# Kernel optimization log

Hardware: AMD Instinct MI355X
Metric: run time of the kernel (lower is better)

## Reference

```python
import jax, jax.numpy as jnp
import numpy as np

BATCH, SEQ, EMBED = 1048576, 1, 32
HIDDEN, LAYERS = 32, 5


def setup_inputs() -> dict:
    key = jax.random.key(0)
    ks = jax.random.split(key, 7)
    s = 1.0 / np.sqrt(HIDDEN)  # PyTorch-style uniform-ish scale via scaled normals
    return {
        "x": jax.random.normal(ks[0], (BATCH, SEQ, EMBED), dtype=jnp.float32),
        "w_ih": jax.random.normal(ks[1], (LAYERS, 3 * HIDDEN, EMBED), dtype=jnp.float32) * s,
        "w_hh": jax.random.normal(ks[2], (LAYERS, 3 * HIDDEN, HIDDEN), dtype=jnp.float32) * s,
        "b_ih": jax.random.normal(ks[3], (LAYERS, 3 * HIDDEN), dtype=jnp.float32) * s,
        "b_hh": jax.random.normal(ks[4], (LAYERS, 3 * HIDDEN), dtype=jnp.float32) * s,
        "fc_w": jax.random.normal(ks[5], (EMBED, HIDDEN)) * s,  # Linear(hidden, embed): (out, in)
        "fc_b": jax.random.normal(ks[6], (EMBED,)) * s,
    }


def _gru_layer(x_tbh, h0, w_ih_l, w_hh_l, b_ih_l, b_hh_l):
    """x_tbh: (T, B, in). Returns all hidden states (T, B, H)."""
    def step(h, x_t):
        gi = x_t @ w_ih_l.T + b_ih_l          # (B, 3H)
        gh = h @ w_hh_l.T + b_hh_l            # (B, 3H)
        i_r, i_z, i_n = jnp.split(gi, 3, axis=-1)
        h_r, h_z, h_n = jnp.split(gh, 3, axis=-1)
        r = jax.nn.sigmoid(i_r + h_r)
        z = jax.nn.sigmoid(i_z + h_z)
        n = jnp.tanh(i_n + r * h_n)
        h_new = (1.0 - z) * n + z * h
        return h_new, h_new
    _, ys = jax.lax.scan(step, h0, x_tbh)
    return ys


def reference(x, w_ih, w_hh, b_ih, b_hh, fc_w, fc_b):
    B = x.shape[0]
    seq = jnp.transpose(x, (1, 0, 2))  # (T, B, E), batch_first -> time-major
    h0 = jnp.zeros((B, HIDDEN), dtype=x.dtype)
    for l in range(LAYERS):  # fixed small layer count
        seq = _gru_layer(seq, h0, w_ih[l], w_hh[l], b_ih[l], b_hh[l])
    out = jnp.transpose(seq, (1, 0, 2)).reshape(B, -1)  # (B, T*H) == (B, H) since T=1
    return out @ fc_w.T + fc_b
```

## Files before the change

### kernel.cpp

```cpp
#include <hip/hip_runtime.h>


typedef __attribute__((ext_vector_type(8))) _Float16 f16x8;
typedef __attribute__((ext_vector_type(4))) float f32x4;
typedef __attribute__((ext_vector_type(2))) float f32x2;
typedef __attribute__((ext_vector_type(4))) unsigned int u32x4;

#define NLAYER 5
#define NT     512

__device__ __forceinline__ float fexp2(float x) {
#if __has_builtin(__builtin_amdgcn_exp2f)
    return __builtin_amdgcn_exp2f(x);
#else
    return exp2f(x);
#endif
}
__device__ __forceinline__ float frcp(float x) {
#if __has_builtin(__builtin_amdgcn_rcpf)
    return __builtin_amdgcn_rcpf(x);
#else
    return 1.0f / x;
#endif
}

__device__ __forceinline__ unsigned cvt2(float f0, float f1) {
    unsigned r;
    asm("v_cvt_pkrtz_f16_f32 %0, %1, %2" : "=v"(r) : "v"(f0), "v"(f1));
    return r;
}

__device__ __forceinline__ f32x4 mfma16h(f16x8 a, f16x8 b, f32x4 c) {
    return __builtin_amdgcn_mfma_f32_16x16x32_f16(a, b, c, 0, 0, 0);
}

__device__ __forceinline__ void xpose_pair(unsigned &x, unsigned &y) {
    asm("v_permlane32_swap_b32 %0, %1" : "+v"(x), "+v"(y));
    asm("v_permlane16_swap_b32 %0, %1" : "+v"(x), "+v"(y));
}

__device__ __forceinline__ f32x2 mk2(float a, float b) { f32x2 v; v.x = a; v.y = b; return v; }
__device__ __forceinline__ f32x2 exp2v(f32x2 v) { f32x2 r; r.x = fexp2(v.x); r.y = fexp2(v.y); return r; }
__device__ __forceinline__ f32x2 rcpv(f32x2 v)  { f32x2 r; r.x = frcp(v.x);  r.y = frcp(v.y);  return r; }

__device__ __forceinline__ f32x2 gru_act2(f32x2 ar, f32x2 az, f32x2 an, f32x2 cn) {
    f32x2 er  = exp2v(ar);
    f32x2 ez  = exp2v(az);
    f32x2 r   = rcpv(er + 1.0f);
    f32x2 a2  = an + r * cn;
    f32x2 en  = exp2v(a2);
    f32x2 num = ez - ez * en;
    f32x2 den = (ez + 1.0f) * (en + 1.0f);
    return num * rcpv(den);
}

struct __align__(16) Lds {
    _Float16 wA[NLAYER * 96 * 32];
    float bsum[NLAYER * 96];
    float cn_[NLAYER * 32];
};

union BU { u32x4 w; f16x8 v; };

__global__ __launch_bounds__(NT, 5) void gru_fused(
    const float* __restrict__ x, const float* __restrict__ w_ih,
    const float* __restrict__ b_ih, const float* __restrict__ b_hh,
    const float* __restrict__ fc_w, const float* __restrict__ fc_b,
    float* __restrict__ out, int nPairs)
{
    __shared__ Lds s;
    const int tid = threadIdx.x;
    const float NL2E = -1.4426950408889634f;

    for (int i = tid; i < NLAYER * 96 * 32; i += NT) {
        int r = i >> 5;
        int g = r % 96;
        float sc = (g < 64) ? NL2E : 2.0f * NL2E;
        s.wA[i ^ ((r & 7) << 3)] = (_Float16)(w_ih[i] * sc);
    }
    for (int i = tid; i < NLAYER * 96; i += NT) {
        int c = i % 96;
        float v = b_ih[i] + (c < 64 ? b_hh[i] : 0.0f);
        s.bsum[i] = v * ((c < 64) ? NL2E : 2.0f * NL2E);
    }
    for (int i = tid; i < NLAYER * 32; i += NT) {
        int l = i >> 5, c = i & 31;
        s.cn_[i] = b_hh[l * 96 + 64 + c] * (2.0f * NL2E);
    }
    __syncthreads();

    const int lane = tid & 63;
    const int n0 = lane & 15;
    const int q  = lane >> 4;
    const int aBase = ((n0 * 32) + q * 8) ^ ((n0 & 7) << 3);

    f16x8 F0, F1;
    {
        const float* p0 = fc_w + (size_t)(n0 * 32 + q * 8);
        const float* p1 = fc_w + (size_t)((16 + n0) * 32 + q * 8);
        f32x4 a0 = *(const f32x4*)p0, a1 = *(const f32x4*)(p0 + 4);
        f32x4 b0 = *(const f32x4*)p1, b1 = *(const f32x4*)(p1 + 4);
        BU U0, U1;
        U0.w[0] = cvt2(a0[0], a0[1]); U0.w[1] = cvt2(a0[2], a0[3]);
        U0.w[2] = cvt2(a1[0], a1[1]); U0.w[3] = cvt2(a1[2], a1[3]);
        U1.w[0] = cvt2(b0[0], b0[1]); U1.w[1] = cvt2(b0[2], b0[3]);
        U1.w[2] = cvt2(b1[0], b1[1]); U1.w[3] = cvt2(b1[2], b1[3]);
        F0 = U0.v; F1 = U1.v;
    }
    f32x4 OB0 = *(const f32x4*)(fc_b + q * 4);
    f32x4 OB1 = *(const f32x4*)(fc_b + 16 + q * 4);

    const int waveId  = (int)((blockIdx.x * (unsigned)NT + tid) >> 6);
    const int nWavesG = (int)((gridDim.x * (unsigned)NT) >> 6);

    for (int t = waveId; t < nPairs; t += nWavesG) {
        const int rowBase = t * 32;

        const float* xpA = x + (size_t)(rowBase + n0) * 32 + q * 8;
        const float* xpB = x + (size_t)(rowBase + 16 + n0) * 32 + q * 8;
        f32x4 xaA = *(const f32x4*)xpA, xbA = *(const f32x4*)(xpA + 4);
        f32x4 xaB = *(const f32x4*)xpB, xbB = *(const f32x4*)(xpB + 4);
        BU BA, BB;
        BA.w[0] = cvt2(xaA[0], xaA[1]); BA.w[1] = cvt2(xaA[2], xaA[3]);
        BA.w[2] = cvt2(xbA[0], xbA[1]); BA.w[3] = cvt2(xbA[2], xbA[3]);
        BB.w[0] = cvt2(xaB[0], xaB[1]); BB.w[1] = cvt2(xaB[2], xaB[3]);
        BB.w[2] = cvt2(xbB[0], xbB[1]); BB.w[3] = cvt2(xbB[2], xbB[3]);
        f16x8 bA = BA.v, bB = BB.v;

        #pragma unroll
        for (int l = 0; l < NLAYER; ++l) {
            const _Float16* wb = s.wA + l * 96 * 32;
            const float* bs = s.bsum + l * 96;

            f32x4 cR0A, cR1A, cZ0A, cZ1A, cN0A, cN1A;
            f32x4 cR0B, cR1B, cZ0B, cZ1B, cN0B, cN1B;

            {
                f16x8 a = *(const f16x8*)(wb + aBase + 0 * 512);
                f32x4 cb = *(const f32x4*)(bs + 0 + q * 4);
                cR0A = mfma16h(a, bA, cb);
                cR0B = mfma16h(a, bB, cb);
            }
            {
                f16x8 a = *(const f16x8*)(wb + aBase + 1 * 512);
                f32x4 cb = *(const f32x4*)(bs + 16 + q * 4);
                cR1A = mfma16h(a, bA, cb);
                cR1B = mfma16h(a, bB, cb);
            }
            {
                f16x8 a = *(const f16x8*)(wb + aBase + 2 * 512);
                f32x4 cb = *(const f32x4*)(bs + 32 + q * 4);
                cZ0A = mfma16h(a, bA, cb);
                cZ0B = mfma16h(a, bB, cb);
            }
            {
                f16x8 a = *(const f16x8*)(wb + aBase + 3 * 512);
                f32x4 cb = *(const f32x4*)(bs + 48 + q * 4);
                cZ1A = mfma16h(a, bA, cb);
                cZ1B = mfma16h(a, bB, cb);
            }
            {
                f16x8 a = *(const f16x8*)(wb + aBase + 4 * 512);
                f32x4 cb = *(const f32x4*)(bs + 64 + q * 4);
                cN0A = mfma16h(a, bA, cb);
                cN0B = mfma16h(a, bB, cb);
            }
            {
                f16x8 a = *(const f16x8*)(wb + aBase + 5 * 512);
                f32x4 cb = *(const f32x4*)(bs + 80 + q * 4);
                cN1A = mfma16h(a, bA, cb);
                cN1B = mfma16h(a, bB, cb);
            }

            f32x4 vc0 = *(const f32x4*)(s.cn_ + l * 32 + 0  + q * 4);
            f32x4 vc1 = *(const f32x4*)(s.cn_ + l * 32 + 16 + q * 4);

            {
                f32x2 hA = gru_act2(mk2(cR0A[0], cR0A[1]), mk2(cZ0A[0], cZ0A[1]),
                                    mk2(cN0A[0], cN0A[1]), mk2(vc0[0], vc0[1]));
                f32x2 hB = gru_act2(mk2(cR0A[2], cR0A[3]), mk2(cZ0A[2], cZ0A[3]),
                                    mk2(cN0A[2], cN0A[3]), mk2(vc0[2], vc0[3]));
                f32x2 hC = gru_act2(mk2(cR1A[0], cR1A[1]), mk2(cZ1A[0], cZ1A[1]),
                                    mk2(cN1A[0], cN1A[1]), mk2(vc1[0], vc1[1]));
                f32x2 hD = gru_act2(mk2(cR1A[2], cR1A[3]), mk2(cZ1A[2], cZ1A[3]),
                                    mk2(cN1A[2], cN1A[3]), mk2(vc1[2], vc1[3]));
                unsigned hw0 = cvt2(hA.x, hA.y);
                unsigned hw1 = cvt2(hB.x, hB.y);
                unsigned hw2 = cvt2(hC.x, hC.y);
                unsigned hw3 = cvt2(hD.x, hD.y);
                xpose_pair(hw0, hw2);
                xpose_pair(hw1, hw3);
                BA.w[0] = hw0; BA.w[1] = hw1; BA.w[2] = hw2; BA.w[3] = hw3;
                bA = BA.v;
            }
            {
                f32x2 hA = gru_act2(mk2(cR0B[0], cR0B[1]), mk2(cZ0B[0], cZ0B[1]),
                                    mk2(cN0B[0], cN0B[1]), mk2(vc0[0], vc0[1]));
                f32x2 hB = gru_act2(mk2(cR0B[2], cR0B[3]), mk2(cZ0B[2], cZ0B[3]),
                                    mk2(cN0B[2], cN0B[3]), mk2(vc0[2], vc0[3]));
                f32x2 hC = gru_act2(mk2(cR1B[0], cR1B[1]), mk2(cZ1B[0], cZ1B[1]),
                                    mk2(cN1B[0], cN1B[1]), mk2(vc1[0], vc1[1]));
                f32x2 hD = gru_act2(mk2(cR1B[2], cR1B[3]), mk2(cZ1B[2], cZ1B[3]),
                                    mk2(cN1B[2], cN1B[3]), mk2(vc1[2], vc1[3]));
                unsigned hw0 = cvt2(hA.x, hA.y);
                unsigned hw1 = cvt2(hB.x, hB.y);
                unsigned hw2 = cvt2(hC.x, hC.y);
                unsigned hw3 = cvt2(hD.x, hD.y);
                xpose_pair(hw0, hw2);
                xpose_pair(hw1, hw3);
                BB.w[0] = hw0; BB.w[1] = hw1; BB.w[2] = hw2; BB.w[3] = hw3;
                bB = BB.v;
            }
        }

        f32x4 o0A = mfma16h(F0, bA, OB0);
        f32x4 o1A = mfma16h(F1, bA, OB1);
        f32x4 o0B = mfma16h(F0, bB, OB0);
        f32x4 o1B = mfma16h(F1, bB, OB1);

        float* opA = out + (size_t)(rowBase + n0) * 32;
        float* opB = out + (size_t)(rowBase + 16 + n0) * 32;
        *(f32x4*)(opA + 0  + q * 4) = o0A;
        *(f32x4*)(opA + 16 + q * 4) = o1A;
        *(f32x4*)(opB + 0  + q * 4) = o0B;
        *(f32x4*)(opB + 16 + q * 4) = o1B;
    }
}

extern "C" void kernel_launch(void* const* d_in, const int* in_sizes, int n_in,
                              void* d_out, int out_size, void* d_ws, size_t ws_size,
                              hipStream_t stream) {
    (void)n_in; (void)d_ws; (void)ws_size; (void)out_size;
    const float* x    = (const float*)d_in[0];
    const float* w_ih = (const float*)d_in[1];
    const float* b_ih = (const float*)d_in[3];
    const float* b_hh = (const float*)d_in[4];
    const float* fc_w = (const float*)d_in[5];
    const float* fc_b = (const float*)d_in[6];
    float* out = (float*)d_out;

    const int batch  = in_sizes[0] / 32;
    const int nPairs = batch / 32;

    gru_fused<<<1024, NT, 0, stream>>>(x, w_ih, b_ih, b_hh, fc_w, fc_b, out, nPairs);
}
```

Before: 111.0 us.

## Process one 16-row tile per wave and move FC weights to LDS

Each wave now handles one 16-row tile per iteration instead of two interleaved tiles, which halves the accumulator and activation register footprint. Launch bounds rise from 5 to 8 waves-per-EU hint. The FC weights and bias move from per-lane registers into LDS. The aim is to trade the ILP of two independent tiles for higher occupancy. It adds an LDS reload of the FC weights on every tile and loses the overlap between the two tiles' MFMA and transcendental work.

```diff
diff --git a/kernel.cpp b/kernel.cpp
--- a/kernel.cpp
+++ b/kernel.cpp
@@ -56,17 +56,19 @@
 
 struct __align__(16) Lds {
     _Float16 wA[NLAYER * 96 * 32];
+    _Float16 wF[32 * 32];
     float bsum[NLAYER * 96];
     float cn_[NLAYER * 32];
+    float fb_[32];
 };
 
 union BU { u32x4 w; f16x8 v; };
 
-__global__ __launch_bounds__(NT, 5) void gru_fused(
+__global__ __launch_bounds__(NT, 8) void gru_fused(
     const float* __restrict__ x, const float* __restrict__ w_ih,
     const float* __restrict__ b_ih, const float* __restrict__ b_hh,
     const float* __restrict__ fc_w, const float* __restrict__ fc_b,
-    float* __restrict__ out, int nPairs)
+    float* __restrict__ out, int nTiles)
 {
     __shared__ Lds s;
     const int tid = threadIdx.x;
@@ -78,6 +80,10 @@
         float sc = (g < 64) ? NL2E : 2.0f * NL2E;
         s.wA[i ^ ((r & 7) << 3)] = (_Float16)(w_ih[i] * sc);
     }
+    for (int i = tid; i < 32 * 32; i += NT) {
+        int r = i >> 5;
+        s.wF[i ^ ((r & 7) << 3)] = (_Float16)fc_w[i];
+    }
     for (int i = tid; i < NLAYER * 96; i += NT) {
         int c = i % 96;
         float v = b_ih[i] + (c < 64 ? b_hh[i] : 0.0f);
@@ -87,6 +93,7 @@
         int l = i >> 5, c = i & 31;
         s.cn_[i] = b_hh[l * 96 + 64 + c] * (2.0f * NL2E);
     }
+    if (tid < 32) s.fb_[tid] = fc_b[tid];
     __syncthreads();
 
     const int lane = tid & 63;
@@ -94,136 +101,89 @@
     const int q  = lane >> 4;
     const int aBase = ((n0 * 32) + q * 8) ^ ((n0 & 7) << 3);
 
-    f16x8 F0, F1;
-    {
-        const float* p0 = fc_w + (size_t)(n0 * 32 + q * 8);
-        const float* p1 = fc_w + (size_t)((16 + n0) * 32 + q * 8);
-        f32x4 a0 = *(const f32x4*)p0, a1 = *(const f32x4*)(p0 + 4);
-        f32x4 b0 = *(const f32x4*)p1, b1 = *(const f32x4*)(p1 + 4);
-        BU U0, U1;
-        U0.w[0] = cvt2(a0[0], a0[1]); U0.w[1] = cvt2(a0[2], a0[3]);
-        U0.w[2] = cvt2(a1[0], a1[1]); U0.w[3] = cvt2(a1[2], a1[3]);
-        U1.w[0] = cvt2(b0[0], b0[1]); U1.w[1] = cvt2(b0[2], b0[3]);
-        U1.w[2] = cvt2(b1[0], b1[1]); U1.w[3] = cvt2(b1[2], b1[3]);
-        F0 = U0.v; F1 = U1.v;
-    }
-    f32x4 OB0 = *(const f32x4*)(fc_b + q * 4);
-    f32x4 OB1 = *(const f32x4*)(fc_b + 16 + q * 4);
-
     const int waveId  = (int)((blockIdx.x * (unsigned)NT + tid) >> 6);
     const int nWavesG = (int)((gridDim.x * (unsigned)NT) >> 6);
 
-    for (int t = waveId; t < nPairs; t += nWavesG) {
-        const int rowBase = t * 32;
-
-        const float* xpA = x + (size_t)(rowBase + n0) * 32 + q * 8;
-        const float* xpB = x + (size_t)(rowBase + 16 + n0) * 32 + q * 8;
-        f32x4 xaA = *(const f32x4*)xpA, xbA = *(const f32x4*)(xpA + 4);
-        f32x4 xaB = *(const f32x4*)xpB, xbB = *(const f32x4*)(xpB + 4);
-        BU BA, BB;
-        BA.w[0] = cvt2(xaA[0], xaA[1]); BA.w[1] = cvt2(xaA[2], xaA[3]);
-        BA.w[2] = cvt2(xbA[0], xbA[1]); BA.w[3] = cvt2(xbA[2], xbA[3]);
-        BB.w[0] = cvt2(xaB[0], xaB[1]); BB.w[1] = cvt2(xaB[2], xaB[3]);
-        BB.w[2] = cvt2(xbB[0], xbB[1]); BB.w[3] = cvt2(xbB[2], xbB[3]);
-        f16x8 bA = BA.v, bB = BB.v;
+    for (int t = waveId; t < nTiles; t += nWavesG) {
+        const int rowBase = t * 16;
+
+        const float* xp = x + (size_t)(rowBase + n0) * 32 + q * 8;
+        f32x4 xa = *(const f32x4*)xp;
+        f32x4 xb = *(const f32x4*)(xp + 4);
+        BU B;
+        B.w[0] = cvt2(xa[0], xa[1]); B.w[1] = cvt2(xa[2], xa[3]);
+        B.w[2] = cvt2(xb[0], xb[1]); B.w[3] = cvt2(xb[2], xb[3]);
+        f16x8 bA = B.v;
 
         #pragma unroll
         for (int l = 0; l < NLAYER; ++l) {
             const _Float16* wb = s.wA + l * 96 * 32;
             const float* bs = s.bsum + l * 96;
 
-            f32x4 cR0A, cR1A, cZ0A, cZ1A, cN0A, cN1A;
-            f32x4 cR0B, cR1B, cZ0B, cZ1B, cN0B, cN1B;
-
+            f32x4 c0, c1, c2, c3, c4, c5;
             {
                 f16x8 a = *(const f16x8*)(wb + aBase + 0 * 512);
                 f32x4 cb = *(const f32x4*)(bs + 0 + q * 4);
-                cR0A = mfma16h(a, bA, cb);
-                cR0B = mfma16h(a, bB, cb);
+                c0 = mfma16h(a, bA, cb);
             }
             {
                 f16x8 a = *(const f16x8*)(wb + aBase + 1 * 512);
                 f32x4 cb = *(const f32x4*)(bs + 16 + q * 4);
-                cR1A = mfma16h(a, bA, cb);
-                cR1B = mfma16h(a, bB, cb);
+                c1 = mfma16h(a, bA, cb);
             }
             {
                 f16x8 a = *(const f16x8*)(wb + aBase + 2 * 512);
                 f32x4 cb = *(const f32x4*)(bs + 32 + q * 4);
-                cZ0A = mfma16h(a, bA, cb);
-                cZ0B = mfma16h(a, bB, cb);
+                c2 = mfma16h(a, bA, cb);
             }
             {
                 f16x8 a = *(const f16x8*)(wb + aBase + 3 * 512);
                 f32x4 cb = *(const f32x4*)(bs + 48 + q * 4);
-                cZ1A = mfma16h(a, bA, cb);
-                cZ1B = mfma16h(a, bB, cb);
+                c3 = mfma16h(a, bA, cb);
             }
             {
                 f16x8 a = *(const f16x8*)(wb + aBase + 4 * 512);
                 f32x4 cb = *(const f32x4*)(bs + 64 + q * 4);
-                cN0A = mfma16h(a, bA, cb);
-                cN0B = mfma16h(a, bB, cb);
+                c4 = mfma16h(a, bA, cb);
             }
             {
                 f16x8 a = *(const f16x8*)(wb + aBase + 5 * 512);
                 f32x4 cb = *(const f32x4*)(bs + 80 + q * 4);
-                cN1A = mfma16h(a, bA, cb);
-                cN1B = mfma16h(a, bB, cb);
+                c5 = mfma16h(a, bA, cb);
             }
 
             f32x4 vc0 = *(const f32x4*)(s.cn_ + l * 32 + 0  + q * 4);
             f32x4 vc1 = *(const f32x4*)(s.cn_ + l * 32 + 16 + q * 4);
 
-            {
-                f32x2 hA = gru_act2(mk2(cR0A[0], cR0A[1]), mk2(cZ0A[0], cZ0A[1]),
-                                    mk2(cN0A[0], cN0A[1]), mk2(vc0[0], vc0[1]));
-                f32x2 hB = gru_act2(mk2(cR0A[2], cR0A[3]), mk2(cZ0A[2], cZ0A[3]),
-                                    mk2(cN0A[2], cN0A[3]), mk2(vc0[2], vc0[3]));
-                f32x2 hC = gru_act2(mk2(cR1A[0], cR1A[1]), mk2(cZ1A[0], cZ1A[1]),
-                                    mk2(cN1A[0], cN1A[1]), mk2(vc1[0], vc1[1]));
-                f32x2 hD = gru_act2(mk2(cR1A[2], cR1A[3]), mk2(cZ1A[2], cZ1A[3]),
-                                    mk2(cN1A[2], cN1A[3]), mk2(vc1[2], vc1[3]));
-                unsigned hw0 = cvt2(hA.x, hA.y);
-                unsigned hw1 = cvt2(hB.x, hB.y);
-                unsigned hw2 = cvt2(hC.x, hC.y);
-                unsigned hw3 = cvt2(hD.x, hD.y);
-                xpose_pair(hw0, hw2);
-                xpose_pair(hw1, hw3);
-                BA.w[0] = hw0; BA.w[1] = hw1; BA.w[2] = hw2; BA.w[3] = hw3;
-                bA = BA.v;
-            }
-            {
-                f32x2 hA = gru_act2(mk2(cR0B[0], cR0B[1]), mk2(cZ0B[0], cZ0B[1]),
-                                    mk2(cN0B[0], cN0B[1]), mk2(vc0[0], vc0[1]));
-                f32x2 hB = gru_act2(mk2(cR0B[2], cR0B[3]), mk2(cZ0B[2], cZ0B[3]),
-                                    mk2(cN0B[2], cN0B[3]), mk2(vc0[2], vc0[3]));
-                f32x2 hC = gru_act2(mk2(cR1B[0], cR1B[1]), mk2(cZ1B[0], cZ1B[1]),
-                                    mk2(cN1B[0], cN1B[1]), mk2(vc1[0], vc1[1]));
-                f32x2 hD = gru_act2(mk2(cR1B[2], cR1B[3]), mk2(cZ1B[2], cZ1B[3]),
-                                    mk2(cN1B[2], cN1B[3]), mk2(vc1[2], vc1[3]));
-                unsigned hw0 = cvt2(hA.x, hA.y);
-                unsigned hw1 = cvt2(hB.x, hB.y);
-                unsigned hw2 = cvt2(hC.x, hC.y);
-                unsigned hw3 = cvt2(hD.x, hD.y);
-                xpose_pair(hw0, hw2);
-                xpose_pair(hw1, hw3);
-                BB.w[0] = hw0; BB.w[1] = hw1; BB.w[2] = hw2; BB.w[3] = hw3;
-                bB = BB.v;
-            }
+            f32x2 hA = gru_act2(mk2(c0[0], c0[1]), mk2(c2[0], c2[1]),
+                                mk2(c4[0], c4[1]), mk2(vc0[0], vc0[1]));
+            f32x2 hB = gru_act2(mk2(c0[2], c0[3]), mk2(c2[2], c2[3]),
+                                mk2(c4[2], c4[3]), mk2(vc0[2], vc0[3]));
+            f32x2 hC = gru_act2(mk2(c1[0], c1[1]), mk2(c3[0], c3[1]),
+                                mk2(c5[0], c5[1]), mk2(vc1[0], vc1[1]));
+            f32x2 hD = gru_act2(mk2(c1[2], c1[3]), mk2(c3[2], c3[3]),
+                                mk2(c5[2], c5[3]), mk2(vc1[2], vc1[3]));
+
+            unsigned hw0 = cvt2(hA.x, hA.y);
+            unsigned hw1 = cvt2(hB.x, hB.y);
+            unsigned hw2 = cvt2(hC.x, hC.y);
+            unsigned hw3 = cvt2(hD.x, hD.y);
+            xpose_pair(hw0, hw2);
+            xpose_pair(hw1, hw3);
+            B.w[0] = hw0; B.w[1] = hw1; B.w[2] = hw2; B.w[3] = hw3;
+            bA = B.v;
         }
 
-        f32x4 o0A = mfma16h(F0, bA, OB0);
-        f32x4 o1A = mfma16h(F1, bA, OB1);
-        f32x4 o0B = mfma16h(F0, bB, OB0);
-        f32x4 o1B = mfma16h(F1, bB, OB1);
-
-        float* opA = out + (size_t)(rowBase + n0) * 32;
-        float* opB = out + (size_t)(rowBase + 16 + n0) * 32;
-        *(f32x4*)(opA + 0  + q * 4) = o0A;
-        *(f32x4*)(opA + 16 + q * 4) = o1A;
-        *(f32x4*)(opB + 0  + q * 4) = o0B;
-        *(f32x4*)(opB + 16 + q * 4) = o1B;
+        f16x8 f0 = *(const f16x8*)(s.wF + aBase);
+        f16x8 f1 = *(const f16x8*)(s.wF + aBase + 512);
+        f32x4 ob0 = *(const f32x4*)(s.fb_ + 0  + q * 4);
+        f32x4 ob1 = *(const f32x4*)(s.fb_ + 16 + q * 4);
+        f32x4 o0 = mfma16h(f0, bA, ob0);
+        f32x4 o1 = mfma16h(f1, bA, ob1);
+
+        float* op = out + (size_t)(rowBase + n0) * 32;
+        *(f32x4*)(op + 0  + q * 4) = o0;
+        *(f32x4*)(op + 16 + q * 4) = o1;
     }
 }
 
@@ -240,7 +200,7 @@
     float* out = (float*)d_out;
 
     const int batch  = in_sizes[0] / 32;
-    const int nPairs = batch / 32;
-
-    gru_fused<<<1024, NT, 0, stream>>>(x, w_ih, b_ih, b_hh, fc_w, fc_b, out, nPairs);
-}
+    const int nTiles = batch / 16;
+
+    gru_fused<<<1024, NT, 0, stream>>>(x, w_ih, b_ih, b_hh, fc_w, fc_b, out, nTiles);
+}
```

Result: no change. 108.8 us (-2.0%).
